# Optimization experiments

Measured on AMD Instinct MI355X. Metric: run time of the kernel, lower is better.

## Reference

```python
import jax, jax.numpy as jnp
import numpy as np

MAX_NUM_ATOMS = 128  # static stand-in for tf's data-dependent max(pair_indices)+1


def setup_inputs() -> dict:
    key = jax.random.key(0)
    k1, k2 = jax.random.split(key)
    B, M, F = 32, 4096, 64
    edge_features = jax.random.normal(k1, (B, M, F), dtype=jnp.float32)
    pair_indices = jax.random.randint(k2, (B, M, 2), 0, MAX_NUM_ATOMS).astype(jnp.int64)
    return {"edge_features": edge_features, "pair_indices": pair_indices}


def reference(edge_features, pair_indices):
    # edge_features: [B, M, F]; pair_indices: [B, M, 2] with values in [0, N)
    B, M, F = edge_features.shape
    N = MAX_NUM_ATOMS
    b_idx = jnp.broadcast_to(jnp.arange(B)[:, None], (B, M))  # batch index per edge
    i_idx = pair_indices[..., 0]
    j_idx = pair_indices[..., 1]
    out = jnp.zeros((B, N, N, F), dtype=edge_features.dtype)
    # scatter-add each edge feature into dense [B, N, N, F] adjacency-feature tensor
    out = out.at[b_idx, i_idx, j_idx].add(edge_features)
    return out
```

## Files before the change

kernel.cpp:

```cpp
#include <hip/hip_runtime.h>

constexpr int B_DIM   = 32;
constexpr int M_EDGES = 4096;
constexpr int F_DIM   = 64;
constexpr int N_ATOMS = 128;

constexpr int TOTAL_EDGES = B_DIM * M_EDGES;
constexpr int CELLS       = B_DIM * N_ATOMS * N_ATOMS;
constexpr int K_CAP       = 4;
constexpr unsigned int POOL_CAP = 4096;

using f32x4 = __attribute__((ext_vector_type(4))) float;
using u32x4 = __attribute__((ext_vector_type(4))) unsigned int;

__global__ __launch_bounds__(256) void bin_edges_kernel(
    const int*          __restrict__ pair,
    int*                __restrict__ counts,
    unsigned int*       __restrict__ list,
    unsigned int*       __restrict__ pool_cnt,
    unsigned long long* __restrict__ pool)
{
    const int e = blockIdx.x * 256 + threadIdx.x;
    const int2 ij = ((const int2*)pair)[e];
    const int b = e >> 12;

    const int cell = (b << 14) | (ij.x << 7) | ij.y;
    const int pos = atomicAdd(&counts[cell], 1);
    if (pos < K_CAP) {
        list[cell * K_CAP + pos] = (unsigned int)e;
    } else {
        const unsigned int pi = atomicAdd(pool_cnt, 1u);
        if (pi < POOL_CAP)
            pool[pi] = ((unsigned long long)(unsigned int)cell << 32) | (unsigned int)e;
    }
}

__global__ __launch_bounds__(256) void gather_write_kernel(
    const float*              __restrict__ edge,
    const int*                __restrict__ counts,
    const unsigned int*       __restrict__ list,
    const unsigned int*       __restrict__ pool_cnt,
    const unsigned long long* __restrict__ pool,
    float*                    __restrict__ out)
{
    const int tid  = blockIdx.x * 256 + threadIdx.x;
    const int cell = tid >> 4;
    const int q    = tid & 15;

    const int cnt = counts[cell];

    f32x4 acc = (f32x4)0.0f;
    const f32x4* ef = (const f32x4*)edge;

    if (cnt > 0) {
        const u32x4 r = *reinterpret_cast<const u32x4*>(list + (size_t)cell * K_CAP);
        const unsigned int e0 = r.x;
        const unsigned int e1 = cnt > 1 ? r.y : e0;
        const unsigned int e2 = cnt > 2 ? r.z : e0;
        const unsigned int e3 = cnt > 3 ? r.w : e0;

        const f32x4 a0 = ef[(size_t)e0 * 16 + q];
        const f32x4 a1 = ef[(size_t)e1 * 16 + q];
        const f32x4 a2 = ef[(size_t)e2 * 16 + q];
        const f32x4 a3 = ef[(size_t)e3 * 16 + q];

        acc = a0;
        acc += a1 * (cnt > 1 ? 1.0f : 0.0f);
        acc += a2 * (cnt > 2 ? 1.0f : 0.0f);
        acc += a3 * (cnt > 3 ? 1.0f : 0.0f);

        if (cnt > K_CAP) {
            unsigned int pc = *pool_cnt;
            pc = pc > POOL_CAP ? POOL_CAP : pc;
            for (unsigned int t = 0; t < pc; ++t) {
                const unsigned long long ent = pool[t];
                if ((int)(ent >> 32) == cell)
                    acc += ef[(size_t)(unsigned int)ent * 16 + q];
            }
        }
    }

    ((f32x4*)out)[(size_t)cell * 16 + q] = acc;
}

extern "C" void kernel_launch(void* const* d_in, const int* in_sizes, int n_in,
                              void* d_out, int out_size, void* d_ws, size_t ws_size,
                              hipStream_t stream) {
    const float* edge = (const float*)d_in[0];
    const int*   pair = (const int*)d_in[1];
    float*       out  = (float*)d_out;

    char* ws = (char*)d_ws;
    int*                counts   = (int*)ws;
    unsigned int*       pool_cnt = (unsigned int*)(ws + (size_t)CELLS * 4);
    unsigned long long* pool     = (unsigned long long*)(ws + (size_t)CELLS * 4 + 16);
    unsigned int*       list     = (unsigned int*)(ws + (size_t)CELLS * 4 + 65536);

    hipMemsetAsync(ws, 0, (size_t)CELLS * 4 + 16, stream);

    bin_edges_kernel<<<TOTAL_EDGES / 256, 256, 0, stream>>>(pair, counts, list, pool_cnt, pool);

    gather_write_kernel<<<(CELLS * 16) / 256, 256, 0, stream>>>(edge, counts, list, pool_cnt, pool, out);
}
```

Measured before the change: 47.78 us.

## Zero-fill output during binning and skip empty cells in gather

Moves the zeroing of the dense output into the binning kernel, so streaming zero stores overlap with the atomic binning. The gather kernel then returns early for empty cells and writes only occupied cells. This cuts gather-kernel work for the mostly empty adjacency tensor but adds extra write traffic for occupied cells, which are now written twice. The launch count stays the same.

```diff
diff --git a/kernel.cpp b/kernel.cpp
--- a/kernel.cpp
+++ b/kernel.cpp
@@ -13,29 +13,45 @@
 using f32x4 = __attribute__((ext_vector_type(4))) float;
 using u32x4 = __attribute__((ext_vector_type(4))) unsigned int;
 
-__global__ __launch_bounds__(256) void bin_edges_kernel(
+__global__ __launch_bounds__(256) void fill_and_bin_kernel(
     const int*          __restrict__ pair,
     int*                __restrict__ counts,
     unsigned int*       __restrict__ list,
     unsigned int*       __restrict__ pool_cnt,
-    unsigned long long* __restrict__ pool)
+    unsigned long long* __restrict__ pool,
+    float*              __restrict__ out)
 {
-    const int e = blockIdx.x * 256 + threadIdx.x;
-    const int2 ij = ((const int2*)pair)[e];
-    const int b = e >> 12;
+    const int tid = (int)threadIdx.x;
+    const int blk = (int)blockIdx.x;
+    const int gid = blk * 256 + tid;
 
-    const int cell = (b << 14) | (ij.x << 7) | ij.y;
-    const int pos = atomicAdd(&counts[cell], 1);
-    if (pos < K_CAP) {
-        list[cell * K_CAP + pos] = (unsigned int)e;
-    } else {
-        const unsigned int pi = atomicAdd(pool_cnt, 1u);
-        if (pi < POOL_CAP)
-            pool[pi] = ((unsigned long long)(unsigned int)cell << 32) | (unsigned int)e;
+    int  pos  = -1, cell = 0;
+    if (gid < TOTAL_EDGES) {
+        const int2 ij = ((const int2*)pair)[gid];
+        const int b = gid >> 12;
+        cell = (b << 14) | (ij.x << 7) | ij.y;
+        pos  = atomicAdd(&counts[cell], 1);
+    }
+
+    f32x4* o4 = (f32x4*)out + (size_t)blk * 8192;
+    const f32x4 z = (f32x4)0.0f;
+    #pragma unroll
+    for (int k = 0; k < 32; ++k)
+        o4[k * 256 + tid] = z;
+
+    if (pos >= 0) {
+        if (pos < K_CAP) {
+            list[cell * K_CAP + pos] = (unsigned int)gid;
+        } else {
+            const unsigned int pi = atomicAdd(pool_cnt, 1u);
+            if (pi < POOL_CAP)
+                pool[pi] = ((unsigned long long)(unsigned int)cell << 32)
+                           | (unsigned int)gid;
+        }
     }
 }
 
-__global__ __launch_bounds__(256) void gather_write_kernel(
+__global__ __launch_bounds__(256) void sparse_gather_kernel(
     const float*              __restrict__ edge,
     const int*                __restrict__ counts,
     const unsigned int*       __restrict__ list,
@@ -48,35 +64,33 @@
     const int q    = tid & 15;
 
     const int cnt = counts[cell];
+    if (cnt <= 0) return;
 
-    f32x4 acc = (f32x4)0.0f;
     const f32x4* ef = (const f32x4*)edge;
 
-    if (cnt > 0) {
-        const u32x4 r = *reinterpret_cast<const u32x4*>(list + (size_t)cell * K_CAP);
-        const unsigned int e0 = r.x;
-        const unsigned int e1 = cnt > 1 ? r.y : e0;
-        const unsigned int e2 = cnt > 2 ? r.z : e0;
-        const unsigned int e3 = cnt > 3 ? r.w : e0;
+    const u32x4 r = *reinterpret_cast<const u32x4*>(list + (size_t)cell * K_CAP);
+    const unsigned int e0 = r.x;
+    const unsigned int e1 = cnt > 1 ? r.y : e0;
+    const unsigned int e2 = cnt > 2 ? r.z : e0;
+    const unsigned int e3 = cnt > 3 ? r.w : e0;
 
-        const f32x4 a0 = ef[(size_t)e0 * 16 + q];
-        const f32x4 a1 = ef[(size_t)e1 * 16 + q];
-        const f32x4 a2 = ef[(size_t)e2 * 16 + q];
-        const f32x4 a3 = ef[(size_t)e3 * 16 + q];
+    const f32x4 a0 = ef[(size_t)e0 * 16 + q];
+    const f32x4 a1 = ef[(size_t)e1 * 16 + q];
+    const f32x4 a2 = ef[(size_t)e2 * 16 + q];
+    const f32x4 a3 = ef[(size_t)e3 * 16 + q];
 
-        acc = a0;
-        acc += a1 * (cnt > 1 ? 1.0f : 0.0f);
-        acc += a2 * (cnt > 2 ? 1.0f : 0.0f);
-        acc += a3 * (cnt > 3 ? 1.0f : 0.0f);
+    f32x4 acc = a0;
+    acc += a1 * (cnt > 1 ? 1.0f : 0.0f);
+    acc += a2 * (cnt > 2 ? 1.0f : 0.0f);
+    acc += a3 * (cnt > 3 ? 1.0f : 0.0f);
 
-        if (cnt > K_CAP) {
-            unsigned int pc = *pool_cnt;
-            pc = pc > POOL_CAP ? POOL_CAP : pc;
-            for (unsigned int t = 0; t < pc; ++t) {
-                const unsigned long long ent = pool[t];
-                if ((int)(ent >> 32) == cell)
-                    acc += ef[(size_t)(unsigned int)ent * 16 + q];
-            }
+    if (cnt > K_CAP) {
+        unsigned int pc = *pool_cnt;
+        pc = pc > POOL_CAP ? POOL_CAP : pc;
+        for (unsigned int t = 0; t < pc; ++t) {
+            const unsigned long long ent = pool[t];
+            if ((int)(ent >> 32) == cell)
+                acc += ef[(size_t)(unsigned int)ent * 16 + q];
         }
     }
 
@@ -98,7 +112,9 @@
 
     hipMemsetAsync(ws, 0, (size_t)CELLS * 4 + 16, stream);
 
-    bin_edges_kernel<<<TOTAL_EDGES / 256, 256, 0, stream>>>(pair, counts, list, pool_cnt, pool);
+    fill_and_bin_kernel<<<1024, 256, 0, stream>>>(pair, counts, list,
+                                                  pool_cnt, pool, out);
 
-    gather_write_kernel<<<(CELLS * 16) / 256, 256, 0, stream>>>(edge, counts, list, pool_cnt, pool, out);
+    sparse_gather_kernel<<<(CELLS * 16) / 256, 256, 0, stream>>>(
+        edge, counts, list, pool_cnt, pool, out);
 }
```

Result: slower. 57.51 us (+20.4%).
